# Optimization experiments

Hardware: AMD Instinct MI355X
Metric: run time of the kernel (lower is better)

## Reference

```python
import jax, jax.numpy as jnp
import numpy as np

B, N, D = 64, 784, 768
H, HD, G = 32, 24, 2
HID = 3072
SCALE = HD ** -0.5
EPS = 1e-6


def _ln(x, g, b):
    m = jnp.mean(x, -1, keepdims=True)
    v = jnp.mean((x - m) ** 2, -1, keepdims=True)
    return (x - m) * jax.lax.rsqrt(v + EPS) * g + b


def setup_inputs() -> dict:
    key = jax.random.key(0)
    ks = jax.random.split(key, 12)
    def rn(k, shape, s=0.02):
        return (jax.random.normal(k, shape) * s).astype(jnp.float32)
    return {
        'x_cls': jax.random.normal(ks[0], (B, 1, D), jnp.float32),
        'x_img': jax.random.normal(ks[1], (B, N, D), jnp.float32),
        'ln1_g': jnp.ones((D,), jnp.float32), 'ln1_b': jnp.zeros((D,), jnp.float32),
        'Wq': rn(ks[2], (D, D)), 'bq': jnp.zeros((D,), jnp.float32),
        'Wk': rn(ks[3], (D, D)), 'bk': jnp.zeros((D,), jnp.float32),
        'Wv': rn(ks[4], (D, D)), 'bv': jnp.zeros((D,), jnp.float32),
        'w1_W': rn(ks[5], (H, H), 0.1), 'w1_b': jnp.zeros((H,), jnp.float32),
        'w2_W': rn(ks[6], (H, H), 0.1), 'w2_b': jnp.zeros((H,), jnp.float32),
        'proj_W': rn(ks[7], (D, D)), 'proj_b': jnp.zeros((D,), jnp.float32),
        'ln2_g': jnp.ones((D,), jnp.float32), 'ln2_b': jnp.zeros((D,), jnp.float32),
        'fc1_W': rn(ks[8], (G, HID // G, D // G)), 'fc1_b': jnp.zeros((G, HID // G), jnp.float32),
        'fc2_W': rn(ks[9], (G, D // G, HID // G)), 'fc2_b': jnp.zeros((G, D // G), jnp.float32),
    }


def reference(x_cls, x_img, ln1_g, ln1_b, Wq, bq, Wk, bk, Wv, bv,
              w1_W, w1_b, w2_W, w2_b, proj_W, proj_b, ln2_g, ln2_b,
              fc1_W, fc1_b, fc2_W, fc2_b):
    # --- ClassAttention (non-mismatch path), dropout = identity (eval) ---
    u = jnp.concatenate([x_cls, x_img], axis=1)  # [B, M, D], M = N+1
    M = u.shape[1]
    n = _ln(u, ln1_g, ln1_b)
    q = ((n[:, :1] @ Wq + bq).reshape(B, 1, H, HD).transpose(0, 2, 1, 3)) * SCALE  # [B,H,1,HD]
    k = (n @ Wk + bk).reshape(B, M, H, HD).transpose(0, 2, 1, 3)                   # [B,H,M,HD]
    v = (n @ Wv + bv).reshape(B, M, H, HD).transpose(0, 2, 1, 3)
    attn = jnp.einsum('bhqd,bhkd->bhqk', q, k)  # [B,H,1,M]
    # interactive score mixing across heads (w1 pre-softmax, w2 post-softmax)
    attn = attn + jnp.einsum('bhqk,hg->bgqk', attn, w1_W) + w1_b[None, :, None, None]
    attn = jax.nn.softmax(attn, axis=-1)
    attn = attn + jnp.einsum('bhqk,hg->bgqk', attn, w2_W) + w2_b[None, :, None, None]
    o = jnp.einsum('bhqk,bhkd->bhqd', attn, v).transpose(0, 2, 1, 3).reshape(B, 1, D)
    x_cls = x_cls + (o @ proj_W + proj_b)
    # --- GroupConvMlp on the cls token (grouped 1x1 convs + channel shuffle) ---
    y = _ln(x_cls, ln2_g, ln2_b)
    h = jnp.einsum('btgc,goc->btgo', y.reshape(B, 1, G, D // G), fc1_W) + fc1_b  # group-major out channels
    h = jax.nn.gelu(h.reshape(B, 1, HID), approximate=False)
    # channel_shuffle(group=G): out channel b*gc+a = in channel a*G+b
    h = h.reshape(B, 1, HID // G, G).transpose(0, 1, 3, 2).reshape(B, 1, HID)
    z = jnp.einsum('btgc,goc->btgo', h.reshape(B, 1, G, HID // G), fc2_W) + fc2_b
    x_cls = x_cls + z.reshape(B, 1, D)
    return (x_cls, x_img)
```

## Files before the change

kernel.cpp:

```cpp
#include <hip/hip_runtime.h>
#include <hip/hip_bf16.h>
#include <math.h>

#define BB   64
#define NN   784
#define DD   768
#define HH   32
#define HD24 24
#define MM   785
#define HIDN 3072
#define QSCALE 0.20412414523193154f
#define LNEPS 1e-6f

#define WS_Q     0
#define WS_RS    49152
#define WS_RM    100352
#define WS_S1P   151552
#define WS_BQP   163840
#define WS_LMX   176128
#define WS_LSM   184320
#define WS_A2P   192512
#define WS_WMP   200704
#define WS_PS    208896
#define WS_C1    210432
#define WS_H2    259584
#define WS_O     456192
#define WS_E     505344
#define WS_T     2143744
#define WS_ZP    0

typedef __attribute__((ext_vector_type(8))) short bf16x8;
typedef __attribute__((ext_vector_type(4))) float f32x4;

__device__ __forceinline__ unsigned packbf(float a, float b) {
  union { __hip_bfloat162 h2; unsigned u; } cv;
  cv.h2 = __float22bfloat162_rn(make_float2(a, b));
  return cv.u;
}
__device__ __forceinline__ float lo16(unsigned w) { return __uint_as_float(w << 16); }
__device__ __forceinline__ float hi16(unsigned w) { return __uint_as_float(w & 0xffff0000u); }

__global__ __launch_bounds__(256) void k_q(
    const float* __restrict__ x_cls,
    const float* __restrict__ g1, const float* __restrict__ b1,
    const float* __restrict__ Wq, const float* __restrict__ bq,
    float* __restrict__ ws)
{
  const int b = blockIdx.y;
  const int oc0 = blockIdx.x * 64;
  const int t = threadIdx.x;
  const int lane = t & 63, wid = t >> 6;

  __shared__ __align__(16) float nc_l[DD];
  __shared__ float red4[4][64];
  __shared__ float rS[4], rQ[4];
  __shared__ float musd[2];

  float xv[3];
  float s = 0.f, q2 = 0.f;
#pragma unroll
  for (int k = 0; k < 3; ++k) {
    float v = x_cls[(size_t)b * DD + t + 256 * k];
    xv[k] = v; s += v; q2 += v * v;
  }
#pragma unroll
  for (int off = 1; off < 64; off <<= 1) { s += __shfl_xor(s, off); q2 += __shfl_xor(q2, off); }
  if (lane == 0) { rS[wid] = s; rQ[wid] = q2; }
  __syncthreads();
  if (t == 0) {
    float ss = rS[0] + rS[1] + rS[2] + rS[3];
    float qq = rQ[0] + rQ[1] + rQ[2] + rQ[3];
    float mu = ss * (1.f / DD);
    musd[0] = mu; musd[1] = rsqrtf(qq * (1.f / DD) - mu * mu + LNEPS);
  }
  __syncthreads();
  {
    float mu = musd[0], rs = musd[1];
#pragma unroll
    for (int k = 0; k < 3; ++k) {
      int d = t + 256 * k;
      nc_l[d] = (xv[k] - mu) * rs * g1[d] + b1[d];
    }
  }
  __syncthreads();

  const int oc = t & 63, ks = t >> 6;
  const float* wp = Wq + (size_t)(ks * 192) * DD + oc0 + oc;
  const float* ncp = nc_l + ks * 192;
  float a0 = 0.f, a1 = 0.f, a2 = 0.f, a3 = 0.f;
#pragma unroll 4
  for (int d = 0; d < 192; d += 4) {
    a0 += ncp[d + 0] * wp[(size_t)(d + 0) * DD];
    a1 += ncp[d + 1] * wp[(size_t)(d + 1) * DD];
    a2 += ncp[d + 2] * wp[(size_t)(d + 2) * DD];
    a3 += ncp[d + 3] * wp[(size_t)(d + 3) * DD];
  }
  red4[ks][oc] = (a0 + a1) + (a2 + a3);
  __syncthreads();
  if (t < 64) {
    int ocg = oc0 + t;
    ws[WS_Q + (size_t)b * DD + ocg] =
        (red4[0][t] + red4[1][t] + red4[2][t] + red4[3][t] + bq[ocg]) * QSCALE;
  }
}

__global__ __launch_bounds__(256) void k_gqk(
    const float* __restrict__ g1, const float* __restrict__ b1,
    const float* __restrict__ Wk, const float* __restrict__ w1W,
    float* __restrict__ ws)
{
  const int b = blockIdx.y;
  const int d0 = blockIdx.x * 128;
  const int t = threadIdx.x;

  __shared__ __align__(16) float q_l[DD];
  __shared__ float T1[HH * HH];
  __shared__ float qk_l[128][33];
  __shared__ float pS[8][HH], pB[8][HH];

  for (int i = t; i < DD; i += 256) q_l[i] = ws[WS_Q + (size_t)b * DD + i];
  for (int i = t; i < HH * HH; i += 256) {
    int g = i >> 5, h = i & 31;
    T1[i] = w1W[i] + ((g == h) ? 1.f : 0.f);
  }
  __syncthreads();

  {
    const int dl = t >> 1, gh = t & 1;
    const float4* wr = (const float4*)(Wk + (size_t)(d0 + dl) * DD + gh * 384);
    const float4* qr = (const float4*)(q_l + gh * 384);
#pragma unroll 4
    for (int gg = 0; gg < 16; ++gg) {
      float a = 0.f;
#pragma unroll
      for (int c = 0; c < 6; ++c) {
        float4 w = wr[gg * 6 + c];
        float4 p = qr[gg * 6 + c];
        a += w.x * p.x + w.y * p.y + w.z * p.z + w.w * p.w;
      }
      qk_l[dl][gh * 16 + gg] = a;
    }
  }
  __syncthreads();
  {
    const int h = t & 31, dg = t >> 5;
    float fb[16];
    float s1a = 0.f, bqa = 0.f;
#pragma unroll 2
    for (int dd = 0; dd < 16; ++dd) {
      int dl = dg * 16 + dd;
      float f = 0.f;
#pragma unroll 8
      for (int g = 0; g < HH; ++g) f += qk_l[dl][g] * T1[g * HH + h];
      float gq = g1[d0 + dl] * f;
      fb[dd] = gq;
      s1a += gq;
      bqa += b1[d0 + dl] * qk_l[dl][h];
    }
    const int kstep = (d0 >> 5) + (dg >> 1);
    const int nt = h >> 4;
    const int lane0 = (h & 15) + 32 * (dg & 1);
    uint4* GQB = (uint4*)(ws + WS_E) + (size_t)b * (24 * 2 * 64);
    GQB[(kstep * 2 + nt) * 64 + lane0] =
        make_uint4(packbf(fb[0], fb[1]), packbf(fb[2], fb[3]),
                   packbf(fb[4], fb[5]), packbf(fb[6], fb[7]));
    GQB[(kstep * 2 + nt) * 64 + lane0 + 16] =
        make_uint4(packbf(fb[8], fb[9]), packbf(fb[10], fb[11]),
                   packbf(fb[12], fb[13]), packbf(fb[14], fb[15]));
    pS[dg][h] = s1a; pB[dg][h] = bqa;
  }
  __syncthreads();
  if (t < HH) {
    float s = 0.f, bq = 0.f;
#pragma unroll
    for (int k = 0; k < 8; ++k) { s += pS[k][t]; bq += pB[k][t]; }
    ws[WS_S1P + ((size_t)b * 6 + blockIdx.x) * HH + t] = s;
    ws[WS_BQP + ((size_t)b * 6 + blockIdx.x) * HH + t] = bq;
  }
}

__global__ __launch_bounds__(256) void k_main1(
    const float* __restrict__ x_cls, const float* __restrict__ x_img,
    float* __restrict__ out, float* __restrict__ ws)
{
  const int b = blockIdx.y;
  const int m0 = blockIdx.x * 64;
  const int t = threadIdx.x;
  const int w = t >> 6;
  const int l = t & 63;
  const int lg = l >> 4;
  const int lm = l & 15;

  const uint4* GQ = (const uint4*)(ws + WS_E) + (size_t)b * (24 * 2 * 64);
  float* out_img = out + (size_t)BB * DD;

  const int arow = m0 + w * 16 + lm;
  const bool av = (arow < MM);
  const int arc = av ? arow : 0;
  const float* asrc = (arc == 0) ? (x_cls + (size_t)b * DD)
                                 : (x_img + ((size_t)b * NN + (arc - 1)) * DD);
  const int koff_l = 8 * lg;

  f32x4 acc0 = {0.f, 0.f, 0.f, 0.f};
  f32x4 acc1 = {0.f, 0.f, 0.f, 0.f};
  float sl = 0.f, sq = 0.f;

#pragma unroll 1
  for (int kc = 0; kc < 12; ++kc) {
#pragma unroll
    for (int p = 0; p < 4; ++p) {
      int i = p * 256 + t;
      int crow = m0 + (i >> 4);
      int cc = i & 15;
      if (crow < MM) {
        const float* src = (crow == 0) ? (x_cls + (size_t)b * DD)
                                       : (x_img + ((size_t)b * NN + (crow - 1)) * DD);
        float4 v = *(const float4*)(src + kc * 64 + cc * 4);
        if (crow >= 1)
          *(float4*)(out_img + ((size_t)b * NN + (crow - 1)) * DD + kc * 64 + cc * 4) = v;
      }
    }
#pragma unroll
    for (int s = 0; s < 2; ++s) {
      const int kst = kc * 2 + s;
      float4 a0 = make_float4(0.f, 0.f, 0.f, 0.f);
      float4 a1 = make_float4(0.f, 0.f, 0.f, 0.f);
      if (av) {
        a0 = *(const float4*)(asrc + kst * 32 + koff_l);
        a1 = *(const float4*)(asrc + kst * 32 + koff_l + 4);
      }
      sl += (a0.x + a0.y) + (a0.z + a0.w) + (a1.x + a1.y) + (a1.z + a1.w);
      sq += a0.x*a0.x + a0.y*a0.y + a0.z*a0.z + a0.w*a0.w
          + a1.x*a1.x + a1.y*a1.y + a1.z*a1.z + a1.w*a1.w;
      union { uint4 u; bf16x8 h; } ua, ub0, ub1;
      ua.u = make_uint4(packbf(a0.x, a0.y), packbf(a0.z, a0.w),
                        packbf(a1.x, a1.y), packbf(a1.z, a1.w));
      ub0.u = GQ[(kst * 2 + 0) * 64 + l];
      ub1.u = GQ[(kst * 2 + 1) * 64 + l];
      acc0 = __builtin_amdgcn_mfma_f32_16x16x32_bf16(ua.h, ub0.h, acc0, 0, 0, 0);
      acc1 = __builtin_amdgcn_mfma_f32_16x16x32_bf16(ua.h, ub1.h, acc1, 0, 0, 0);
    }
  }

  sl += __shfl_xor(sl, 16); sl += __shfl_xor(sl, 32);
  sq += __shfl_xor(sq, 16); sq += __shfl_xor(sq, 32);
  if (lg == 0 && av) {
    float mu = sl * (1.f / DD);
    float rs = rsqrtf(sq * (1.f / DD) - mu * mu + LNEPS);
    ws[WS_RS + (size_t)b * 800 + arow] = rs;
    ws[WS_RM + (size_t)b * 800 + arow] = rs * mu;
  }

  float* tb = ws + WS_T + (size_t)b * MM * HH;
#pragma unroll
  for (int r = 0; r < 4; ++r) {
    int row = m0 + w * 16 + 4 * lg + r;
    if (row < MM) {
      tb[(size_t)row * HH + lm] = acc0[r];
      tb[(size_t)row * HH + 16 + lm] = acc1[r];
    }
  }
}

__global__ __launch_bounds__(256) void k_sm_a(
    const float* __restrict__ bk,
    const float* __restrict__ w1W, const float* __restrict__ w1b,
    float* __restrict__ ws)
{
  const int cx = blockIdx.x, b = blockIdx.y;
  const int t = threadIdx.x;
  const int lane = t & 63, wid = t >> 6;

  __shared__ float T1[HH * HH];
  __shared__ float s1_sh[HH], c0_sh[HH], bq_sh[HH];
  __shared__ float red[4][HH];
  __shared__ float lmax_sh[HH];

  for (int i = t; i < HH * HH; i += 256) {
    int g = i >> 5, h = i & 31;
    T1[i] = w1W[i] + ((g == h) ? 1.f : 0.f);
  }
  if (t < HH) {
    float s1v = 0.f, bqv = 0.f;
#pragma unroll
    for (int p = 0; p < 6; ++p) {
      s1v += ws[WS_S1P + ((size_t)b * 6 + p) * HH + t];
      bqv += ws[WS_BQP + ((size_t)b * 6 + p) * HH + t];
    }
    const float* qp = ws + WS_Q + (size_t)b * DD + t * HD24;
#pragma unroll
    for (int j = 0; j < HD24; ++j) bqv += bk[t * HD24 + j] * qp[j];
    s1_sh[t] = s1v; bq_sh[t] = bqv;
  }
  __syncthreads();
  if (t < HH) {
    float c0 = w1b[t];
#pragma unroll
    for (int g = 0; g < HH; ++g) c0 += T1[g * HH + t] * bq_sh[g];
    c0_sh[t] = c0;
  }
  __syncthreads();

  const int m = cx * 256 + t;
  const bool vm = (m < MM);
  float a1[HH];
  if (vm) {
    const float* tb = ws + WS_T + ((size_t)b * MM + m) * HH;
    float rs = ws[WS_RS + (size_t)b * 800 + m];
    float rm = ws[WS_RM + (size_t)b * 800 + m];
#pragma unroll
    for (int q = 0; q < 8; ++q) {
      float4 tv = *(const float4*)(tb + q * 4);
      a1[4*q+0] = rs * tv.x - rm * s1_sh[4*q+0] + c0_sh[4*q+0];
      a1[4*q+1] = rs * tv.y - rm * s1_sh[4*q+1] + c0_sh[4*q+1];
      a1[4*q+2] = rs * tv.z - rm * s1_sh[4*q+2] + c0_sh[4*q+2];
      a1[4*q+3] = rs * tv.w - rm * s1_sh[4*q+3] + c0_sh[4*q+3];
    }
  } else {
#pragma unroll
    for (int h = 0; h < HH; ++h) a1[h] = -3.0e38f;
  }
#pragma unroll
  for (int h = 0; h < HH; ++h) {
    float v = a1[h];
#pragma unroll
    for (int off = 1; off < 64; off <<= 1) v = fmaxf(v, __shfl_xor(v, off));
    if (lane == 0) red[wid][h] = v;
  }
  __syncthreads();
  if (t < HH) {
    float v = fmaxf(fmaxf(red[0][t], red[1][t]), fmaxf(red[2][t], red[3][t]));
    lmax_sh[t] = v;
    ws[WS_LMX + ((size_t)b * 4 + cx) * HH + t] = v;
  }
  __syncthreads();
  float* E = ws + WS_E + (size_t)b * (HH * 800);
  if (vm) {
#pragma unroll
    for (int h = 0; h < HH; ++h) {
      float e = __expf(a1[h] - lmax_sh[h]);
      a1[h] = e;
      E[(size_t)h * 800 + m] = e;
    }
  } else {
#pragma unroll
    for (int h = 0; h < HH; ++h) a1[h] = 0.f;
  }
#pragma unroll
  for (int h = 0; h < HH; ++h) {
    float v = a1[h];
#pragma unroll
    for (int off = 1; off < 64; off <<= 1) v += __shfl_xor(v, off);
    if (lane == 0) red[wid][h] = v;
  }
  __syncthreads();
  if (t < HH)
    ws[WS_LSM + ((size_t)b * 4 + cx) * HH + t] = red[0][t] + red[1][t] + red[2][t] + red[3][t];
}

__global__ __launch_bounds__(256) void k_sm_b(
    const float* __restrict__ w2W, const float* __restrict__ w2b,
    float* __restrict__ ws)
{
  const int cx = blockIdx.x, b = blockIdx.y;
  const int t = threadIdx.x;
  const int lane = t & 63, wid = t >> 6;

  __shared__ __align__(16) float T2s[HH * HH];
  __shared__ float inv_sh[HH], w2b_sh[HH];
  __shared__ float red[4][HH];

  if (t < HH) {
    float l0 = ws[WS_LMX + ((size_t)b * 4 + 0) * HH + t];
    float l1 = ws[WS_LMX + ((size_t)b * 4 + 1) * HH + t];
    float l2 = ws[WS_LMX + ((size_t)b * 4 + 2) * HH + t];
    float l3 = ws[WS_LMX + ((size_t)b * 4 + 3) * HH + t];
    float gmax = fmaxf(fmaxf(l0, l1), fmaxf(l2, l3));
    float s = ws[WS_LSM + ((size_t)b * 4 + 0) * HH + t] * __expf(l0 - gmax)
            + ws[WS_LSM + ((size_t)b * 4 + 1) * HH + t] * __expf(l1 - gmax)
            + ws[WS_LSM + ((size_t)b * 4 + 2) * HH + t] * __expf(l2 - gmax)
            + ws[WS_LSM + ((size_t)b * 4 + 3) * HH + t] * __expf(l3 - gmax);
    float lcx = (cx == 0) ? l0 : (cx == 1) ? l1 : (cx == 2) ? l2 : l3;
    inv_sh[t] = __expf(lcx - gmax) / s;
    w2b_sh[t] = w2b[t];
  }
  __syncthreads();
  for (int i = t; i < HH * HH; i += 256) {
    int g = i >> 5, h = i & 31;
    T2s[i] = (w2W[i] + ((g == h) ? 1.f : 0.f)) * inv_sh[g];
  }
  __syncthreads();

  const int m = cx * 256 + t;
  float* E = ws + WS_E + (size_t)b * (HH * 800);
  float4 av[8];
#pragma unroll
  for (int q = 0; q < 8; ++q) av[q] = make_float4(0.f,0.f,0.f,0.f);
  float rm = 0.f;
  if (m < MM) {
    float rs = ws[WS_RS + (size_t)b * 800 + m];
    rm = ws[WS_RM + (size_t)b * 800 + m];
#pragma unroll 4
    for (int g = 0; g < HH; ++g) {
      float eg = E[(size_t)g * 800 + m];
#pragma unroll
      for (int q = 0; q < 8; ++q) {
        float4 t2 = *(const float4*)&T2s[g * HH + q * 4];
        av[q].x += eg * t2.x; av[q].y += eg * t2.y;
        av[q].z += eg * t2.z; av[q].w += eg * t2.w;
      }
    }
#pragma unroll
    for (int q = 0; q < 8; ++q) {
      av[q].x += w2b_sh[q*4+0]; av[q].y += w2b_sh[q*4+1];
      av[q].z += w2b_sh[q*4+2]; av[q].w += w2b_sh[q*4+3];
      E[(size_t)(q*4+0) * 800 + m] = av[q].x * rs;
      E[(size_t)(q*4+1) * 800 + m] = av[q].y * rs;
      E[(size_t)(q*4+2) * 800 + m] = av[q].z * rs;
      E[(size_t)(q*4+3) * 800 + m] = av[q].w * rs;
    }
  } else if (m < 800) {
#pragma unroll
    for (int h = 0; h < HH; ++h) E[(size_t)h * 800 + m] = 0.f;
  }
#pragma unroll
  for (int h = 0; h < HH; ++h) {
    float v = ((const float*)&av[h >> 2])[h & 3];
#pragma unroll
    for (int off = 1; off < 64; off <<= 1) v += __shfl_xor(v, off);
    if (lane == 0) red[wid][h] = v;
  }
  __syncthreads();
  if (t < HH)
    ws[WS_A2P + ((size_t)b * 4 + cx) * HH + t] = red[0][t] + red[1][t] + red[2][t] + red[3][t];
  __syncthreads();
#pragma unroll
  for (int h = 0; h < HH; ++h) {
    float v = ((const float*)&av[h >> 2])[h & 3] * rm;
#pragma unroll
    for (int off = 1; off < 64; off <<= 1) v += __shfl_xor(v, off);
    if (lane == 0) red[wid][h] = v;
  }
  __syncthreads();
  if (t < HH)
    ws[WS_WMP + ((size_t)b * 4 + cx) * HH + t] = red[0][t] + red[1][t] + red[2][t] + red[3][t];
}

__global__ __launch_bounds__(256) void k_wsum(
    const float* __restrict__ x_cls, const float* __restrict__ x_img,
    float* __restrict__ ws)
{
  const int b = blockIdx.y;
  const int d0 = blockIdx.x * 64;
  const int t = threadIdx.x;
  const int dseg = t & 15;
  const int msub = (t >> 4) & 3;
  const int hb = (t >> 6) * 8;

  __shared__ __align__(16) float w_s[HH][36];
  const float* W = ws + WS_E + (size_t)b * (HH * 800);

  float acc[8][4];
#pragma unroll
  for (int j = 0; j < 8; ++j)
#pragma unroll
    for (int c = 0; c < 4; ++c) acc[j][c] = 0.f;

  float4 pu[8], pun[8];
  float4 pwn;

  auto LOADU = [&](int mc, float4* dst) {
#pragma unroll
    for (int i = 0; i < 8; ++i) {
      int m = mc * 32 + msub * 8 + i;
      if (m < MM) {
        const float* src = (m == 0) ? (x_cls + (size_t)b * DD)
                                    : (x_img + ((size_t)b * NN + (m - 1)) * DD);
        dst[i] = *(const float4*)(src + d0 + dseg * 4);
      } else dst[i] = make_float4(0.f,0.f,0.f,0.f);
    }
  };

  LOADU(0, pu);
  {
    float4 pw = *(const float4*)(W + (size_t)(t >> 3) * 800 + (t & 7) * 4);
    *(float4*)&w_s[t >> 3][(t & 7) * 4] = pw;
  }
  __syncthreads();

  for (int mc = 0; mc < 25; ++mc) {
    if (mc < 24) {
      pwn = *(const float4*)(W + (size_t)(t >> 3) * 800 + (mc + 1) * 32 + (t & 7) * 4);
      LOADU(mc + 1, pun);
    }
#pragma unroll
    for (int j = 0; j < 8; ++j) {
      float4 wA = *(const float4*)&w_s[hb + j][msub * 8];
      float4 wB = *(const float4*)&w_s[hb + j][msub * 8 + 4];
      float wv0 = wA.x, wv1 = wA.y, wv2 = wA.z, wv3 = wA.w;
      float wv4 = wB.x, wv5 = wB.y, wv6 = wB.z, wv7 = wB.w;
      acc[j][0] += wv0*pu[0].x + wv1*pu[1].x + wv2*pu[2].x + wv3*pu[3].x
                 + wv4*pu[4].x + wv5*pu[5].x + wv6*pu[6].x + wv7*pu[7].x;
      acc[j][1] += wv0*pu[0].y + wv1*pu[1].y + wv2*pu[2].y + wv3*pu[3].y
                 + wv4*pu[4].y + wv5*pu[5].y + wv6*pu[6].y + wv7*pu[7].y;
      acc[j][2] += wv0*pu[0].z + wv1*pu[1].z + wv2*pu[2].z + wv3*pu[3].z
                 + wv4*pu[4].z + wv5*pu[5].z + wv6*pu[6].z + wv7*pu[7].z;
      acc[j][3] += wv0*pu[0].w + wv1*pu[1].w + wv2*pu[2].w + wv3*pu[3].w
                 + wv4*pu[4].w + wv5*pu[5].w + wv6*pu[6].w + wv7*pu[7].w;
    }
    __syncthreads();
    if (mc < 24) {
      *(float4*)&w_s[t >> 3][(t & 7) * 4] = pwn;
#pragma unroll
      for (int i = 0; i < 8; ++i) pu[i] = pun[i];
    }
    __syncthreads();
  }

#pragma unroll
  for (int j = 0; j < 8; ++j)
#pragma unroll
    for (int c = 0; c < 4; ++c) {
      float v = acc[j][c];
      v += __shfl_xor(v, 16);
      v += __shfl_xor(v, 32);
      acc[j][c] = v;
    }
  if (msub == 0) {
    float* R = ws + WS_T + (size_t)b * HH * DD;
#pragma unroll
    for (int j = 0; j < 8; ++j)
      *(float4*)(R + (size_t)(hb + j) * DD + d0 + dseg * 4) =
          make_float4(acc[j][0], acc[j][1], acc[j][2], acc[j][3]);
  }
}

__global__ __launch_bounds__(192) void k_att_o(
    const float* __restrict__ g1, const float* __restrict__ b1,
    const float* __restrict__ Wv, const float* __restrict__ bv,
    float* __restrict__ ws)
{
  const int h = blockIdx.x;
  const int b = blockIdx.y;
  const int t = threadIdx.x;

  __shared__ __align__(16) float agg_l[DD];
  __shared__ float red[8][25];
  __shared__ float a2wm[2];

  if (t == 0) {
    float a = 0.f;
#pragma unroll
    for (int c = 0; c < 4; ++c) a += ws[WS_A2P + ((size_t)b * 4 + c) * HH + h];
    a2wm[0] = a;
  }
  if (t == 1) {
    float w = 0.f;
#pragma unroll
    for (int c = 0; c < 4; ++c) w += ws[WS_WMP + ((size_t)b * 4 + c) * HH + h];
    a2wm[1] = w;
  }
  __syncthreads();
  const float A2 = a2wm[0], WM = a2wm[1];
  const float* R = ws + WS_T + ((size_t)b * HH + h) * DD;
  for (int i = t; i < DD; i += 192)
    agg_l[i] = g1[i] * (R[i] - WM) + b1[i] * A2;
  __syncthreads();

  const int oc = t % 24, ks = t / 24;
  const float* wv = Wv + (size_t)(ks * 96) * DD + h * HD24 + oc;
  const float* ag = agg_l + ks * 96;
  float a0 = 0.f, a1 = 0.f, a2 = 0.f, a3 = 0.f;
#pragma unroll 4
  for (int d = 0; d < 96; d += 4) {
    a0 += ag[d + 0] * wv[(size_t)(d + 0) * DD];
    a1 += ag[d + 1] * wv[(size_t)(d + 1) * DD];
    a2 += ag[d + 2] * wv[(size_t)(d + 2) * DD];
    a3 += ag[d + 3] * wv[(size_t)(d + 3) * DD];
  }
  red[ks][oc] = (a0 + a1) + (a2 + a3);
  __syncthreads();
  if (t < 24) {
    float o = A2 * bv[h * HD24 + t];
#pragma unroll
    for (int k = 0; k < 8; ++k) o += red[k][t];
    ws[WS_O + (size_t)b * DD + h * HD24 + t] = o;
  }
}

__global__ __launch_bounds__(256) void k_proj2(
    const float* __restrict__ x_cls,
    const float* __restrict__ projW, const float* __restrict__ projb,
    float* __restrict__ ws)
{
  const int b = blockIdx.y;
  const int oc0 = blockIdx.x * 64;
  const int t = threadIdx.x;

  __shared__ __align__(16) float o_l[DD];
  __shared__ float red4[4][64];

  for (int i = t; i < DD; i += 256) o_l[i] = ws[WS_O + (size_t)b * DD + i];
  __syncthreads();

  const int oc = t & 63, ks = t >> 6;
  const float* wp = projW + (size_t)(ks * 192) * DD + oc0 + oc;
  const float* op = o_l + ks * 192;
  float a0 = 0.f, a1 = 0.f, a2 = 0.f, a3 = 0.f;
#pragma unroll 4
  for (int d = 0; d < 192; d += 4) {
    a0 += op[d + 0] * wp[(size_t)(d + 0) * DD];
    a1 += op[d + 1] * wp[(size_t)(d + 1) * DD];
    a2 += op[d + 2] * wp[(size_t)(d + 2) * DD];
    a3 += op[d + 3] * wp[(size_t)(d + 3) * DD];
  }
  red4[ks][oc] = (a0 + a1) + (a2 + a3);
  __syncthreads();
  if (t < 64) {
    int ocg = oc0 + t;
    float c1 = red4[0][t] + red4[1][t] + red4[2][t] + red4[3][t]
             + projb[ocg] + x_cls[(size_t)b * DD + ocg];
    ws[WS_C1 + (size_t)b * DD + ocg] = c1;
    float cs = c1, cq = c1 * c1;
#pragma unroll
    for (int off = 1; off < 64; off <<= 1) { cs += __shfl_xor(cs, off); cq += __shfl_xor(cq, off); }
    if (t == 0) {
      ws[WS_PS + ((size_t)b * 12 + blockIdx.x) * 2 + 0] = cs;
      ws[WS_PS + ((size_t)b * 12 + blockIdx.x) * 2 + 1] = cq;
    }
  }
}

__global__ __launch_bounds__(256) void k_fc1(
    const float* __restrict__ fc1W, const float* __restrict__ fc1b,
    const float* __restrict__ g2, const float* __restrict__ b2,
    float* __restrict__ ws)
{
  const int g = blockIdx.x / 48;
  const int oc0 = (blockIdx.x % 48) * 32;
  const int t = threadIdx.x;
  const int txo = t & 7, tyb = t >> 3;

  __shared__ float y_s[64][65];
  __shared__ float w_s[32][65];
  __shared__ float mv[64][2];

  if (t < 64) {
    float s = 0.f, q = 0.f;
#pragma unroll
    for (int p = 0; p < 12; ++p) {
      s += ws[WS_PS + ((size_t)t * 12 + p) * 2 + 0];
      q += ws[WS_PS + ((size_t)t * 12 + p) * 2 + 1];
    }
    float mu = s * (1.f / DD);
    mv[t][0] = mu;
    mv[t][1] = rsqrtf(q * (1.f / DD) - mu * mu + LNEPS);
  }
  __syncthreads();

  float acc[2][4];
#pragma unroll
  for (int i = 0; i < 2; ++i)
#pragma unroll
    for (int j = 0; j < 4; ++j) acc[i][j] = 0.f;

#pragma unroll 1
  for (int kc = 0; kc < 6; ++kc) {
    {
      int r = t >> 2;
      float mu = mv[r][0], rs = mv[r][1];
#pragma unroll
      for (int p = 0; p < 4; ++p) {
        int c = (t & 3) * 4 + p * 16;
        int gc = g * 384 + kc * 64 + c;
        float4 v = *(const float4*)(ws + WS_C1 + (size_t)r * DD + gc);
        float4 gg = *(const float4*)(g2 + gc);
        float4 bb = *(const float4*)(b2 + gc);
        y_s[r][c+0] = (v.x - mu) * rs * gg.x + bb.x;
        y_s[r][c+1] = (v.y - mu) * rs * gg.y + bb.y;
        y_s[r][c+2] = (v.z - mu) * rs * gg.z + bb.z;
        y_s[r][c+3] = (v.w - mu) * rs * gg.w + bb.w;
      }
      int rw = t >> 3;
#pragma unroll
      for (int p = 0; p < 2; ++p) {
        int c = (t & 7) * 4 + p * 32;
        float4 w = *(const float4*)(fc1W + ((size_t)(g * 1536 + oc0 + rw)) * 384 + kc * 64 + c);
        w_s[rw][c+0] = w.x; w_s[rw][c+1] = w.y; w_s[rw][c+2] = w.z; w_s[rw][c+3] = w.w;
      }
    }
    __syncthreads();
#pragma unroll 4
    for (int kk = 0; kk < 64; ++kk) {
      float y0 = y_s[2*tyb+0][kk], y1 = y_s[2*tyb+1][kk];
      float w0 = w_s[4*txo+0][kk], w1 = w_s[4*txo+1][kk];
      float w2 = w_s[4*txo+2][kk], w3 = w_s[4*txo+3][kk];
      acc[0][0] += y0*w0; acc[0][1] += y0*w1; acc[0][2] += y0*w2; acc[0][3] += y0*w3;
      acc[1][0] += y1*w0; acc[1][1] += y1*w1; acc[1][2] += y1*w2; acc[1][3] += y1*w3;
    }
    __syncthreads();
  }

  float* H2 = ws + WS_H2;
#pragma unroll
  for (int i = 0; i < 2; ++i) {
    int bb = 2 * tyb + i;
#pragma unroll
    for (int j = 0; j < 4; ++j) {
      int oc = oc0 + 4 * txo + j;
      float v = acc[i][j] + fc1b[g * 1536 + oc];
      v = 0.5f * v * (1.f + erff(v * 0.70710678118654752f));
      H2[(size_t)bb * HIDN + (oc & 1) * 1536 + g * 768 + (oc >> 1)] = v;
    }
  }
}

__global__ __launch_bounds__(256) void k_fc2(
    const float* __restrict__ fc2W, float* __restrict__ ws)
{
  const int oc0 = blockIdx.x * 32;
  const int kq = blockIdx.y;
  const int g = blockIdx.z;
  const int t = threadIdx.x;
  const int txo = t & 7, tyb = t >> 3;

  __shared__ float h_s[64][65];
  __shared__ float w_s[32][65];

  float acc[2][4];
#pragma unroll
  for (int i = 0; i < 2; ++i)
#pragma unroll
    for (int j = 0; j < 4; ++j) acc[i][j] = 0.f;

  const float* H2 = ws + WS_H2;

#pragma unroll 1
  for (int kc = 0; kc < 6; ++kc) {
    {
      int r = t >> 2;
#pragma unroll
      for (int p = 0; p < 4; ++p) {
        int c = (t & 3) * 4 + p * 16;
        float4 v = *(const float4*)(H2 + (size_t)r * HIDN + g * 1536 + kq * 384 + kc * 64 + c);
        h_s[r][c+0] = v.x; h_s[r][c+1] = v.y; h_s[r][c+2] = v.z; h_s[r][c+3] = v.w;
      }
      int rw = t >> 3;
#pragma unroll
      for (int p = 0; p < 2; ++p) {
        int c = (t & 7) * 4 + p * 32;
        float4 w = *(const float4*)(fc2W + ((size_t)(g * 384 + oc0 + rw)) * 1536 + kq * 384 + kc * 64 + c);
        w_s[rw][c+0] = w.x; w_s[rw][c+1] = w.y; w_s[rw][c+2] = w.z; w_s[rw][c+3] = w.w;
      }
    }
    __syncthreads();
#pragma unroll 4
    for (int kk = 0; kk < 64; ++kk) {
      float y0 = h_s[2*tyb+0][kk], y1 = h_s[2*tyb+1][kk];
      float w0 = w_s[4*txo+0][kk], w1 = w_s[4*txo+1][kk];
      float w2 = w_s[4*txo+2][kk], w3 = w_s[4*txo+3][kk];
      acc[0][0] += y0*w0; acc[0][1] += y0*w1; acc[0][2] += y0*w2; acc[0][3] += y0*w3;
      acc[1][0] += y1*w0; acc[1][1] += y1*w1; acc[1][2] += y1*w2; acc[1][3] += y1*w3;
    }
    __syncthreads();
  }

  float* ZP = ws + WS_ZP + (size_t)kq * BB * DD;
#pragma unroll
  for (int i = 0; i < 2; ++i)
#pragma unroll
    for (int j = 0; j < 4; ++j)
      ZP[(size_t)(2 * tyb + i) * DD + g * 384 + oc0 + 4 * txo + j] = acc[i][j];
}

__global__ __launch_bounds__(256) void k_final(
    const float* __restrict__ fc2b, float* __restrict__ out, const float* __restrict__ ws)
{
  int idx = blockIdx.x * 256 + threadIdx.x;
  int d = idx % DD;
  float v = ws[WS_C1 + idx] + fc2b[d];
#pragma unroll
  for (int kq = 0; kq < 4; ++kq) v += ws[WS_ZP + (size_t)kq * BB * DD + idx];
  out[idx] = v;
}

extern "C" void kernel_launch(void* const* d_in, const int* in_sizes, int n_in,
                              void* d_out, int out_size, void* d_ws, size_t ws_size,
                              hipStream_t stream)
{
  (void)in_sizes; (void)n_in; (void)out_size; (void)ws_size;
  const float* x_cls = (const float*)d_in[0];
  const float* x_img = (const float*)d_in[1];
  const float* ln1_g = (const float*)d_in[2];
  const float* ln1_b = (const float*)d_in[3];
  const float* Wq    = (const float*)d_in[4];
  const float* bq    = (const float*)d_in[5];
  const float* Wk    = (const float*)d_in[6];
  const float* bk    = (const float*)d_in[7];
  const float* Wv    = (const float*)d_in[8];
  const float* bv    = (const float*)d_in[9];
  const float* w1W   = (const float*)d_in[10];
  const float* w1b   = (const float*)d_in[11];
  const float* w2W   = (const float*)d_in[12];
  const float* w2b   = (const float*)d_in[13];
  const float* projW = (const float*)d_in[14];
  const float* projb = (const float*)d_in[15];
  const float* ln2_g = (const float*)d_in[16];
  const float* ln2_b = (const float*)d_in[17];
  const float* fc1W  = (const float*)d_in[18];
  const float* fc1b  = (const float*)d_in[19];
  const float* fc2W  = (const float*)d_in[20];
  const float* fc2b  = (const float*)d_in[21];
  float* out = (float*)d_out;
  float* ws  = (float*)d_ws;

  k_q    <<<dim3(12, 64), dim3(256), 0, stream>>>(x_cls, ln1_g, ln1_b, Wq, bq, ws);
  k_gqk  <<<dim3(6, 64),  dim3(256), 0, stream>>>(ln1_g, ln1_b, Wk, w1W, ws);
  k_main1<<<dim3(13, 64), dim3(256), 0, stream>>>(x_cls, x_img, out, ws);
  k_sm_a <<<dim3(4, 64),  dim3(256), 0, stream>>>(bk, w1W, w1b, ws);
  k_sm_b <<<dim3(4, 64),  dim3(256), 0, stream>>>(w2W, w2b, ws);
  k_wsum <<<dim3(12, 64), dim3(256), 0, stream>>>(x_cls, x_img, ws);
  k_att_o<<<dim3(32, 64), dim3(192), 0, stream>>>(ln1_g, ln1_b, Wv, bv, ws);
  k_proj2<<<dim3(12, 64), dim3(256), 0, stream>>>(x_cls, projW, projb, ws);
  k_fc1  <<<dim3(96),     dim3(256), 0, stream>>>(fc1W, fc1b, ln2_g, ln2_b, ws);
  k_fc2  <<<dim3(12, 4, 2), dim3(256), 0, stream>>>(fc2W, ws);
  k_final<<<dim3(192),    dim3(256), 0, stream>>>(fc2b, out, ws);
}
```

Baseline: 320.4 us.

## Split K reduction across two wave halves in main and wsum kernels

k_main1 and k_wsum now launch 512 threads per block. In each, two halves of the block process separate halves of the reduction dimension (K for main1, M chunks for wsum) and their partial sums are combined through shared memory. k_main1 also double-buffers the x_img copy to out with register prefetch and uses nontemporal stores. The aim is more memory-level parallelism and latency hiding on these bandwidth-heavy passes, at the cost of extra shared memory, a barrier, and possible register pressure under the higher launch bound.

```diff
diff --git a/kernel.cpp b/kernel.cpp
--- a/kernel.cpp
+++ b/kernel.cpp
@@ -37,8 +37,6 @@
   cv.h2 = __float22bfloat162_rn(make_float2(a, b));
   return cv.u;
 }
-__device__ __forceinline__ float lo16(unsigned w) { return __uint_as_float(w << 16); }
-__device__ __forceinline__ float hi16(unsigned w) { return __uint_as_float(w & 0xffff0000u); }
 
 __global__ __launch_bounds__(256) void k_q(
     const float* __restrict__ x_cls,
@@ -179,7 +177,7 @@
   }
 }
 
-__global__ __launch_bounds__(256) void k_main1(
+__global__ __launch_bounds__(512) void k_main1(
     const float* __restrict__ x_cls, const float* __restrict__ x_img,
     float* __restrict__ out, float* __restrict__ ws)
 {
@@ -188,46 +186,69 @@
   const int t = threadIdx.x;
   const int w = t >> 6;
   const int l = t & 63;
+  const int kh = w >> 2;
+  const int wl = w & 3;
   const int lg = l >> 4;
   const int lm = l & 15;
+  const int ci = t & 255;
+
+  __shared__ float ts[64][33];
+  __shared__ float ssl[64], ssq[64];
 
   const uint4* GQ = (const uint4*)(ws + WS_E) + (size_t)b * (24 * 2 * 64);
   float* out_img = out + (size_t)BB * DD;
 
-  const int arow = m0 + w * 16 + lm;
+  const int arow = m0 + wl * 16 + lm;
   const bool av = (arow < MM);
   const int arc = av ? arow : 0;
   const float* asrc = (arc == 0) ? (x_cls + (size_t)b * DD)
                                  : (x_img + ((size_t)b * NN + (arc - 1)) * DD);
-  const int koff_l = 8 * lg;
+  const int kbase = kh * 384;
+
+  float4 pfA[4], pfB[4];
+  auto CLOAD = [&](float4* pf, int kc) {
+#pragma unroll
+    for (int p = 0; p < 4; ++p) {
+      int ii = p * 256 + ci;
+      int row = m0 + (ii >> 4);
+      if (row < MM) {
+        const float* src = (row == 0) ? (x_cls + (size_t)b * DD)
+                                      : (x_img + ((size_t)b * NN + (row - 1)) * DD);
+        pf[p] = *(const float4*)(src + kbase + kc * 64 + (ii & 15) * 4);
+      } else pf[p] = make_float4(0.f, 0.f, 0.f, 0.f);
+    }
+  };
+  auto CSTORE = [&](float4* pf, int kc) {
+#pragma unroll
+    for (int p = 0; p < 4; ++p) {
+      int ii = p * 256 + ci;
+      int row = m0 + (ii >> 4);
+      if (row >= 1 && row < MM) {
+        f32x4 v = { pf[p].x, pf[p].y, pf[p].z, pf[p].w };
+        __builtin_nontemporal_store(v,
+            (f32x4*)(out_img + ((size_t)b * NN + (row - 1)) * DD + kbase + kc * 64 + (ii & 15) * 4));
+      }
+    }
+  };
 
   f32x4 acc0 = {0.f, 0.f, 0.f, 0.f};
   f32x4 acc1 = {0.f, 0.f, 0.f, 0.f};
   float sl = 0.f, sq = 0.f;
 
+  CLOAD(pfA, 0);
 #pragma unroll 1
-  for (int kc = 0; kc < 12; ++kc) {
-#pragma unroll
-    for (int p = 0; p < 4; ++p) {
-      int i = p * 256 + t;
-      int crow = m0 + (i >> 4);
-      int cc = i & 15;
-      if (crow < MM) {
-        const float* src = (crow == 0) ? (x_cls + (size_t)b * DD)
-                                       : (x_img + ((size_t)b * NN + (crow - 1)) * DD);
-        float4 v = *(const float4*)(src + kc * 64 + cc * 4);
-        if (crow >= 1)
-          *(float4*)(out_img + ((size_t)b * NN + (crow - 1)) * DD + kc * 64 + cc * 4) = v;
-      }
-    }
+  for (int kc = 0; kc < 6; ++kc) {
+    float4* cur = (kc & 1) ? pfB : pfA;
+    float4* nxt = (kc & 1) ? pfA : pfB;
+    if (kc < 5) CLOAD(nxt, kc + 1);
 #pragma unroll
     for (int s = 0; s < 2; ++s) {
-      const int kst = kc * 2 + s;
+      const int kst = kh * 12 + kc * 2 + s;
       float4 a0 = make_float4(0.f, 0.f, 0.f, 0.f);
       float4 a1 = make_float4(0.f, 0.f, 0.f, 0.f);
       if (av) {
-        a0 = *(const float4*)(asrc + kst * 32 + koff_l);
-        a1 = *(const float4*)(asrc + kst * 32 + koff_l + 4);
+        a0 = *(const float4*)(asrc + kst * 32 + 8 * lg);
+        a1 = *(const float4*)(asrc + kst * 32 + 8 * lg + 4);
       }
       sl += (a0.x + a0.y) + (a0.z + a0.w) + (a1.x + a1.y) + (a1.z + a1.w);
       sq += a0.x*a0.x + a0.y*a0.y + a0.z*a0.z + a0.w*a0.w
@@ -240,24 +261,40 @@
       acc0 = __builtin_amdgcn_mfma_f32_16x16x32_bf16(ua.h, ub0.h, acc0, 0, 0, 0);
       acc1 = __builtin_amdgcn_mfma_f32_16x16x32_bf16(ua.h, ub1.h, acc1, 0, 0, 0);
     }
+    CSTORE(cur, kc);
   }
 
   sl += __shfl_xor(sl, 16); sl += __shfl_xor(sl, 32);
   sq += __shfl_xor(sq, 16); sq += __shfl_xor(sq, 32);
-  if (lg == 0 && av) {
-    float mu = sl * (1.f / DD);
-    float rs = rsqrtf(sq * (1.f / DD) - mu * mu + LNEPS);
-    ws[WS_RS + (size_t)b * 800 + arow] = rs;
-    ws[WS_RM + (size_t)b * 800 + arow] = rs * mu;
-  }
-
-  float* tb = ws + WS_T + (size_t)b * MM * HH;
-#pragma unroll
-  for (int r = 0; r < 4; ++r) {
-    int row = m0 + w * 16 + 4 * lg + r;
-    if (row < MM) {
-      tb[(size_t)row * HH + lm] = acc0[r];
-      tb[(size_t)row * HH + 16 + lm] = acc1[r];
+
+  if (kh == 1) {
+#pragma unroll
+    for (int r = 0; r < 4; ++r) {
+      int rl = wl * 16 + 4 * lg + r;
+      ts[rl][lm] = acc0[r];
+      ts[rl][16 + lm] = acc1[r];
+    }
+    if (lg == 0) { ssl[wl * 16 + lm] = sl; ssq[wl * 16 + lm] = sq; }
+  }
+  __syncthreads();
+  if (kh == 0) {
+    float* tb = ws + WS_T + (size_t)b * MM * HH;
+#pragma unroll
+    for (int r = 0; r < 4; ++r) {
+      int rl = wl * 16 + 4 * lg + r;
+      int row = m0 + rl;
+      if (row < MM) {
+        tb[(size_t)row * HH + lm] = acc0[r] + ts[rl][lm];
+        tb[(size_t)row * HH + 16 + lm] = acc1[r] + ts[rl][16 + lm];
+      }
+    }
+    if (lg == 0 && av) {
+      float slt = sl + ssl[wl * 16 + lm];
+      float sqt = sq + ssq[wl * 16 + lm];
+      float mu = slt * (1.f / DD);
+      float rs = rsqrtf(sqt * (1.f / DD) - mu * mu + LNEPS);
+      ws[WS_RS + (size_t)b * 800 + arow] = rs;
+      ws[WS_RM + (size_t)b * 800 + arow] = rs * mu;
     }
   }
 }
@@ -446,19 +483,28 @@
     ws[WS_WMP + ((size_t)b * 4 + cx) * HH + t] = red[0][t] + red[1][t] + red[2][t] + red[3][t];
 }
 
-__global__ __launch_bounds__(256) void k_wsum(
+__global__ __launch_bounds__(512) void k_wsum(
     const float* __restrict__ x_cls, const float* __restrict__ x_img,
     float* __restrict__ ws)
 {
   const int b = blockIdx.y;
   const int d0 = blockIdx.x * 64;
   const int t = threadIdx.x;
+  const int wv = t >> 6;
+  const int mh = wv >> 2;
+  const int hb = (wv & 3) * 8;
   const int dseg = t & 15;
   const int msub = (t >> 4) & 3;
-  const int hb = (t >> 6) * 8;
-
-  __shared__ __align__(16) float w_s[HH][36];
+  const int mcBeg = mh * 13;
+  const int mcN = 13 - mh;
+
+  __shared__ __align__(16) float w_s[2][HH][36];
+  __shared__ __align__(16) float r_s[HH][68];
+
   const float* W = ws + WS_E + (size_t)b * (HH * 800);
+  const int sh = t >> 8;
+  const int si = t & 255;
+  const int shN = 13 - sh;
 
   float acc[8][4];
 #pragma unroll
@@ -469,11 +515,11 @@
   float4 pu[8], pun[8];
   float4 pwn;
 
-  auto LOADU = [&](int mc, float4* dst) {
+  auto LOADU = [&](int j, float4* dst) {
 #pragma unroll
     for (int i = 0; i < 8; ++i) {
-      int m = mc * 32 + msub * 8 + i;
-      if (m < MM) {
+      int m = (mcBeg + j) * 32 + msub * 8 + i;
+      if (j < mcN && m < MM) {
         const float* src = (m == 0) ? (x_cls + (size_t)b * DD)
                                     : (x_img + ((size_t)b * NN + (m - 1)) * DD);
         dst[i] = *(const float4*)(src + d0 + dseg * 4);
@@ -483,34 +529,38 @@
 
   LOADU(0, pu);
   {
-    float4 pw = *(const float4*)(W + (size_t)(t >> 3) * 800 + (t & 7) * 4);
-    *(float4*)&w_s[t >> 3][(t & 7) * 4] = pw;
-  }
-  __syncthreads();
-
-  for (int mc = 0; mc < 25; ++mc) {
-    if (mc < 24) {
-      pwn = *(const float4*)(W + (size_t)(t >> 3) * 800 + (mc + 1) * 32 + (t & 7) * 4);
-      LOADU(mc + 1, pun);
-    }
-#pragma unroll
-    for (int j = 0; j < 8; ++j) {
-      float4 wA = *(const float4*)&w_s[hb + j][msub * 8];
-      float4 wB = *(const float4*)&w_s[hb + j][msub * 8 + 4];
-      float wv0 = wA.x, wv1 = wA.y, wv2 = wA.z, wv3 = wA.w;
-      float wv4 = wB.x, wv5 = wB.y, wv6 = wB.z, wv7 = wB.w;
-      acc[j][0] += wv0*pu[0].x + wv1*pu[1].x + wv2*pu[2].x + wv3*pu[3].x
-                 + wv4*pu[4].x + wv5*pu[5].x + wv6*pu[6].x + wv7*pu[7].x;
-      acc[j][1] += wv0*pu[0].y + wv1*pu[1].y + wv2*pu[2].y + wv3*pu[3].y
-                 + wv4*pu[4].y + wv5*pu[5].y + wv6*pu[6].y + wv7*pu[7].y;
-      acc[j][2] += wv0*pu[0].z + wv1*pu[1].z + wv2*pu[2].z + wv3*pu[3].z
-                 + wv4*pu[4].z + wv5*pu[5].z + wv6*pu[6].z + wv7*pu[7].z;
-      acc[j][3] += wv0*pu[0].w + wv1*pu[1].w + wv2*pu[2].w + wv3*pu[3].w
-                 + wv4*pu[4].w + wv5*pu[5].w + wv6*pu[6].w + wv7*pu[7].w;
+    float4 pw = *(const float4*)(W + (size_t)(si >> 3) * 800 + (sh * 13) * 32 + (si & 7) * 4);
+    *(float4*)&w_s[sh][si >> 3][(si & 7) * 4] = pw;
+  }
+  __syncthreads();
+
+  for (int j = 0; j < 13; ++j) {
+    if (j + 1 < 13) {
+      if (j + 1 < shN)
+        pwn = *(const float4*)(W + (size_t)(si >> 3) * 800 + (sh * 13 + j + 1) * 32 + (si & 7) * 4);
+      LOADU(j + 1, pun);
+    }
+    if (j < mcN) {
+#pragma unroll
+      for (int jj = 0; jj < 8; ++jj) {
+        float4 wA = *(const float4*)&w_s[mh][hb + jj][msub * 8];
+        float4 wB = *(const float4*)&w_s[mh][hb + jj][msub * 8 + 4];
+        float wv0 = wA.x, wv1 = wA.y, wv2 = wA.z, wv3 = wA.w;
+        float wv4 = wB.x, wv5 = wB.y, wv6 = wB.z, wv7 = wB.w;
+        acc[jj][0] += wv0*pu[0].x + wv1*pu[1].x + wv2*pu[2].x + wv3*pu[3].x
+                    + wv4*pu[4].x + wv5*pu[5].x + wv6*pu[6].x + wv7*pu[7].x;
+        acc[jj][1] += wv0*pu[0].y + wv1*pu[1].y + wv2*pu[2].y + wv3*pu[3].y
+                    + wv4*pu[4].y + wv5*pu[5].y + wv6*pu[6].y + wv7*pu[7].y;
+        acc[jj][2] += wv0*pu[0].z + wv1*pu[1].z + wv2*pu[2].z + wv3*pu[3].z
+                    + wv4*pu[4].z + wv5*pu[5].z + wv6*pu[6].z + wv7*pu[7].z;
+        acc[jj][3] += wv0*pu[0].w + wv1*pu[1].w + wv2*pu[2].w + wv3*pu[3].w
+                    + wv4*pu[4].w + wv5*pu[5].w + wv6*pu[6].w + wv7*pu[7].w;
+      }
     }
     __syncthreads();
-    if (mc < 24) {
-      *(float4*)&w_s[t >> 3][(t & 7) * 4] = pwn;
+    if (j + 1 < 13) {
+      if (j + 1 < shN)
+        *(float4*)&w_s[sh][si >> 3][(si & 7) * 4] = pwn;
 #pragma unroll
       for (int i = 0; i < 8; ++i) pu[i] = pun[i];
     }
@@ -526,12 +576,22 @@
       v += __shfl_xor(v, 32);
       acc[j][c] = v;
     }
-  if (msub == 0) {
+  if (mh == 1 && msub == 0) {
+#pragma unroll
+    for (int j = 0; j < 8; ++j)
+      *(float4*)&r_s[hb + j][dseg * 4] =
+          make_float4(acc[j][0], acc[j][1], acc[j][2], acc[j][3]);
+  }
+  __syncthreads();
+  if (mh == 0 && msub == 0) {
     float* R = ws + WS_T + (size_t)b * HH * DD;
 #pragma unroll
-    for (int j = 0; j < 8; ++j)
+    for (int j = 0; j < 8; ++j) {
+      float4 rv = *(const float4*)&r_s[hb + j][dseg * 4];
       *(float4*)(R + (size_t)(hb + j) * DD + d0 + dseg * 4) =
-          make_float4(acc[j][0], acc[j][1], acc[j][2], acc[j][3]);
+          make_float4(acc[j][0] + rv.x, acc[j][1] + rv.y,
+                      acc[j][2] + rv.z, acc[j][3] + rv.w);
+    }
   }
 }
 
@@ -816,10 +876,10 @@
 
   k_q    <<<dim3(12, 64), dim3(256), 0, stream>>>(x_cls, ln1_g, ln1_b, Wq, bq, ws);
   k_gqk  <<<dim3(6, 64),  dim3(256), 0, stream>>>(ln1_g, ln1_b, Wk, w1W, ws);
-  k_main1<<<dim3(13, 64), dim3(256), 0, stream>>>(x_cls, x_img, out, ws);
+  k_main1<<<dim3(13, 64), dim3(512), 0, stream>>>(x_cls, x_img, out, ws);
   k_sm_a <<<dim3(4, 64),  dim3(256), 0, stream>>>(bk, w1W, w1b, ws);
   k_sm_b <<<dim3(4, 64),  dim3(256), 0, stream>>>(w2W, w2b, ws);
-  k_wsum <<<dim3(12, 64), dim3(256), 0, stream>>>(x_cls, x_img, ws);
+  k_wsum <<<dim3(12, 64), dim3(512), 0, stream>>>(x_cls, x_img, ws);
   k_att_o<<<dim3(32, 64), dim3(192), 0, stream>>>(ln1_g, ln1_b, Wv, bv, ws);
   k_proj2<<<dim3(12, 64), dim3(256), 0, stream>>>(x_cls, projW, projb, ws);
   k_fc1  <<<dim3(96),     dim3(256), 0, stream>>>(fc1W, fc1b, ln2_g, ln2_b, ws);
```

After: 374.0 us. 1.17x slower.
